# Kernel tuning notes

Hardware: AMD Instinct MI355X
Metric: run time of the kernel (lower is better)

Reference implementation:

```python
import jax, jax.numpy as jnp
import numpy as np
import math
from jax import lax

B, NP1, M, D, H, L, DFF = 16, 65, 256, 512, 8, 3, 2048
EPS_PROJ = 0.01  # MartingaleProjectionLayer is built with epsilon=0.01
LN_EPS = 1e-5


def _pos_encoding(n, d):
    pos = np.arange(n, dtype=np.float32)[:, None]
    div = np.exp(np.arange(0, d, 2, dtype=np.float32) * (-math.log(10000.0) / d))
    pe = np.zeros((n, d), dtype=np.float32)
    pe[:, 0::2] = np.sin(pos * div)
    pe[:, 1::2] = np.cos(pos * div)
    return jnp.asarray(pe)


def setup_inputs() -> dict:
    key = jax.random.key(0)
    ks = jax.random.split(key, 32)
    s = 0.02
    marg = jax.random.uniform(ks[0], (B, NP1, M), jnp.float32)
    marg = marg / marg.sum(axis=-1, keepdims=True)  # proper distributions
    return {
        "marginals": marg,
        "x_grid": jnp.linspace(-3.0, 3.0, M, dtype=jnp.float32),
        "conv_w": jax.random.normal(ks[1], (128, 1, 5), jnp.float32) * s,
        "conv_b": jax.random.normal(ks[2], (128,), jnp.float32) * s,
        "fc_w": jax.random.normal(ks[3], (128, D), jnp.float32) * s,
        "fc_b": jax.random.normal(ks[4], (D,), jnp.float32) * s,
        "ln0_g": jnp.ones((D,), jnp.float32),
        "ln0_b": jnp.zeros((D,), jnp.float32),
        "pos_enc": _pos_encoding(NP1, D),
        "qkv_w": jax.random.normal(ks[5], (L, 3 * D, D), jnp.float32) * s,
        "qkv_b": jax.random.normal(ks[6], (L, 3 * D), jnp.float32) * s,
        "out_w": jax.random.normal(ks[7], (L, D, D), jnp.float32) * s,
        "out_b": jax.random.normal(ks[8], (L, D), jnp.float32) * s,
        "ln1_g": jnp.ones((L, D), jnp.float32),
        "ln1_b": jnp.zeros((L, D), jnp.float32),
        "ff1_w": jax.random.normal(ks[9], (L, DFF, D), jnp.float32) * s,
        "ff1_b": jax.random.normal(ks[10], (L, DFF), jnp.float32) * s,
        "ff2_w": jax.random.normal(ks[11], (L, D, DFF), jnp.float32) * s,
        "ff2_b": jax.random.normal(ks[12], (L, D), jnp.float32) * s,
        "ln2_g": jnp.ones((L, D), jnp.float32),
        "ln2_b": jnp.zeros((L, D), jnp.float32),
        "u_w": jax.random.normal(ks[13], (M, D), jnp.float32) * s,
        "u_b": jax.random.normal(ks[14], (M,), jnp.float32) * s,
        "h_w": jax.random.normal(ks[15], (M, D), jnp.float32) * s,
        "h_b": jax.random.normal(ks[16], (M,), jnp.float32) * s,
    }


def _ln(x, g, b):
    mu = x.mean(axis=-1, keepdims=True)
    var = ((x - mu) ** 2).mean(axis=-1, keepdims=True)
    return (x - mu) * lax.rsqrt(var + LN_EPS) * g + b


def _gelu(x):
    return jax.nn.gelu(x, approximate=False)  # torch default exact GELU


def reference(marginals, x_grid, conv_w, conv_b, fc_w, fc_b, ln0_g, ln0_b,
              pos_enc, qkv_w, qkv_b, out_w, out_b, ln1_g, ln1_b,
              ff1_w, ff1_b, ff2_w, ff2_b, ln2_g, ln2_b, u_w, u_b, h_w, h_b):
    b, np1, m = marginals.shape
    n = np1 - 1
    d = fc_w.shape[1]
    nh = H
    dh = d // nh

    # ---- marginal embedding: Conv1d(1,128,k=5,pad=2) -> mean over grid -> FC+LN+GELU
    x = marginals.reshape(b * np1, 1, m)
    y = lax.conv_general_dilated(x, conv_w, (1,), [(2, 2)],
                                 dimension_numbers=("NCH", "OIH", "NCH"))
    y = y + conv_b[None, :, None]          # (b*np1, 128, m)
    emb = y.mean(axis=2)                   # (b*np1, 128)
    emb = _gelu(_ln(emb @ fc_w + fc_b, ln0_g, ln0_b))
    xs = emb.reshape(b, np1, d) + pos_enc[None, :np1, :]

    # ---- post-norm transformer encoder (dropout off / eval mode)
    scale = 1.0 / math.sqrt(dh)
    for l in range(L):
        qkv = xs @ qkv_w[l].T + qkv_b[l]                        # (b, s, 3d)
        q, k, v = jnp.split(qkv, 3, axis=-1)
        q = q.reshape(b, np1, nh, dh).transpose(0, 2, 1, 3)
        k = k.reshape(b, np1, nh, dh).transpose(0, 2, 1, 3)
        v = v.reshape(b, np1, nh, dh).transpose(0, 2, 1, 3)
        att = jax.nn.softmax(jnp.einsum("bhqd,bhkd->bhqk", q, k) * scale, axis=-1)
        o = jnp.einsum("bhqk,bhkd->bhqd", att, v)
        o = o.transpose(0, 2, 1, 3).reshape(b, np1, d)
        o = o @ out_w[l].T + out_b[l]
        xs = _ln(xs + o, ln1_g[l], ln1_b[l])
        ff = _gelu(xs @ ff1_w[l].T + ff1_b[l]) @ ff2_w[l].T + ff2_b[l]
        xs = _ln(xs + ff, ln2_g[l], ln2_b[l])

    u_pot = xs @ u_w.T + u_b                                    # (b, np1, M)
    h_raw = xs[:, :n, :] @ h_w.T + h_b                          # (b, n, M)

    # ---- vectorized martingale projection over all N timesteps
    x_diff = x_grid[:, None] - x_grid[None, :]                  # (M, M)
    h_kernel = h_raw[..., None] * x_diff                        # (b, n, M, M)
    P = jax.nn.softmax(h_kernel / EPS_PROJ, axis=-1)
    expected_next = jnp.einsum("bnij,j->bni", P, x_grid)
    drift = expected_next - x_grid                              # (b, n, M)
    mu = marginals[:, :n, :]
    weight_drift = (mu * drift).sum(axis=-1, keepdims=True)
    correction = weight_drift / (mu.sum(axis=-1, keepdims=True) + 1e-8)
    h_pot = h_raw - correction
    return (u_pot, h_pot)
```

## Files before the change

### kernel.cpp

```cpp
#include <hip/hip_runtime.h>
#include <math.h>


#define BT   1040
#define NP1  65
#define Dm   512
#define MG   256

typedef short short8 __attribute__((ext_vector_type(8)));
typedef float f32x4  __attribute__((ext_vector_type(4)));
typedef unsigned short u16;

__device__ __forceinline__ u16 f2bf(float f) {
  unsigned int u = __float_as_uint(f);
  u += 0x7FFF + ((u >> 16) & 1);
  return (u16)(u >> 16);
}

__device__ __forceinline__ float gelu_exact(float x) {
  return 0.5f * x * (1.0f + erff(x * 0.70710678118654752f));
}

__device__ __forceinline__ void async16(const u16* g, u16* l) {
  __builtin_amdgcn_global_load_lds(
      (const __attribute__((address_space(1))) unsigned int*)g,
      (__attribute__((address_space(3))) unsigned int*)l, 16, 0, 0);
}

__device__ __forceinline__ float wred(float v) {
#pragma unroll
  for (int o = 32; o; o >>= 1) v += __shfl_xor(v, o, 64);
  return v;
}

__device__ __forceinline__ float block_reduce_sum(float v, float* s) {
#pragma unroll
  for (int off = 32; off; off >>= 1) v += __shfl_down(v, off, 64);
  int lane = threadIdx.x & 63, wid = threadIdx.x >> 6;
  __syncthreads();
  if (lane == 0) s[wid] = v;
  __syncthreads();
  return s[0] + s[1] + s[2] + s[3];
}

__device__ __forceinline__ float f_closed(float a) {
  const float tf = 2.3529411765f;
  float t = a * tf;
  float s = fabsf(t);
  float E;
  if (s < 1e-4f) {
    E = 127.5f - 5461.25f * t;
  } else {
    float u = s * 256.0f;
    float term2 = (u < 80.0f) ? 256.0f / expm1f(u) : 0.0f;
    float Epos = 1.0f / expm1f(s) - term2;
    E = (t > 0.0f) ? Epos : 255.0f - Epos;
  }
  return -3.0f + 0.0235294118f * E;
}

__global__ __launch_bounds__(256) void prep_kernel(
    const float* __restrict__ qkv_w, const float* __restrict__ out_w,
    const float* __restrict__ ff1_w, const float* __restrict__ ff2_w,
    const float* __restrict__ u_w,   const float* __restrict__ h_w,
    u16* __restrict__ wdst,
    const float* __restrict__ marg, const float* __restrict__ conv_w,
    const float* __restrict__ conv_b, const float* __restrict__ fc_w,
    const float* __restrict__ fc_b, const float* __restrict__ g,
    const float* __restrict__ bb, const float* __restrict__ pos,
    float* __restrict__ xs, u16* __restrict__ xsb)
{
  const int tid = threadIdx.x;
  if (blockIdx.x < 512) {
    const size_t O1 = 2359296, O2 = 3145728, O3 = 6291456;
    const size_t O4 = 9437184, O5 = 9568256, TOT4 = 9699328 / 4;
    for (size_t e4 = (size_t)blockIdx.x * 256 + tid; e4 < TOT4;
         e4 += (size_t)512 * 256) {
      size_t e = e4 * 4;
      const float* src;
      if      (e < O1) src = qkv_w + e;
      else if (e < O2) src = out_w + (e - O1);
      else if (e < O3) src = ff1_w + (e - O2);
      else if (e < O4) src = ff2_w + (e - O3);
      else if (e < O5) src = u_w   + (e - O4);
      else             src = h_w   + (e - O5);
      float4 v = *(const float4*)src;
      unsigned int lo = (unsigned int)f2bf(v.x) | ((unsigned int)f2bf(v.y) << 16);
      unsigned int hi = (unsigned int)f2bf(v.z) | ((unsigned int)f2bf(v.w) << 16);
      *(uint2*)(wdst + e) = make_uint2(lo, hi);
    }
    return;
  }
  __shared__ float es[4][128];
  __shared__ float sS[4];
  __shared__ float edge[4][4];
  __shared__ float red[4];
  const int t0 = (blockIdx.x - 512) * 4;
  const int lane = tid & 63, wave = tid >> 6;
  {
    float4 mv = *(const float4*)(marg + (size_t)(t0 + wave) * MG + lane * 4);
    float S = wred(mv.x + mv.y + mv.z + mv.w);
    if (lane == 0) sS[wave] = S;
  }
  if (tid < 16) {
    int k = tid >> 2, e = tid & 3;
    int idx = (e < 2) ? e : (e + 252);
    edge[k][e] = marg[(size_t)(t0 + k) * MG + idx];
  }
  __syncthreads();
  if (tid < 128) {
    int o = tid;
    float w0 = conv_w[o*5+0], w1 = conv_w[o*5+1], w2 = conv_w[o*5+2];
    float w3 = conv_w[o*5+3], w4 = conv_w[o*5+4], cb = conv_b[o];
#pragma unroll
    for (int k = 0; k < 4; ++k) {
      float S = sS[k];
      float x0 = edge[k][0], x1 = edge[k][1], x254 = edge[k][2], x255 = edge[k][3];
      es[k][o] = (w0*(S - x254 - x255) + w1*(S - x255) + w2*S
                + w3*(S - x0) + w4*(S - x0 - x1)) * (1.0f/256.0f) + cb;
    }
  }
  __syncthreads();
  float b0 = fc_b[tid], b1 = fc_b[tid + 256];
  float z[4][2];
#pragma unroll
  for (int k = 0; k < 4; ++k) { z[k][0] = b0; z[k][1] = b1; }
#pragma unroll 4
  for (int o = 0; o < 128; ++o) {
    float f0 = fc_w[(size_t)o*Dm + tid];
    float f1 = fc_w[(size_t)o*Dm + tid + 256];
#pragma unroll
    for (int k = 0; k < 4; ++k) {
      float e = es[k][o];
      z[k][0] += e * f0; z[k][1] += e * f1;
    }
  }
  float g0 = g[tid], g1 = g[tid+256], e0 = bb[tid], e1 = bb[tid+256];
#pragma unroll
  for (int k = 0; k < 4; ++k) {
    float mu = block_reduce_sum(z[k][0] + z[k][1], red) * (1.0f/512.0f);
    float d0 = z[k][0] - mu, d1 = z[k][1] - mu;
    float var = block_reduce_sum(d0*d0 + d1*d1, red) * (1.0f/512.0f);
    float inv = rsqrtf(var + 1e-5f);
    int t = t0 + k, p = t % NP1;
    float y0 = gelu_exact(d0*inv*g0 + e0) + pos[(size_t)p*Dm + tid];
    float y1 = gelu_exact(d1*inv*g1 + e1) + pos[(size_t)p*Dm + tid + 256];
    xs[(size_t)t*Dm + tid]        = y0;
    xs[(size_t)t*Dm + tid + 256]  = y1;
    xsb[(size_t)t*Dm + tid]       = f2bf(y0);
    xsb[(size_t)t*Dm + tid + 256] = f2bf(y1);
  }
}

template<int SPLITS, int MODE>
__global__ __launch_bounds__(256) void gemm_mfma(
    const u16* __restrict__ A, const u16* __restrict__ Bw,
    const float* __restrict__ bias, float* __restrict__ Cf,
    u16* __restrict__ Cb, float* __restrict__ C2,
    const float* __restrict__ bias2, int Mrows, int N, int K)
{
  __shared__ u16 Asl[2][8*64*8];
  __shared__ u16 Bsl[2][8*64*8];
  const int tid = threadIdx.x;
  const int row0 = blockIdx.y * 64, col0 = blockIdx.x * 64;
  const int Ks = K / SPLITS, kbase = (int)blockIdx.z * Ks;
  const int lane = tid & 63, wave = tid >> 6;
  const int wm = (wave >> 1) * 32, wn = (wave & 1) * 32;
  const int l15 = lane & 15, q = lane >> 4;

  f32x4 acc[2][2];
  acc[0][0] = (f32x4){0,0,0,0}; acc[0][1] = (f32x4){0,0,0,0};
  acc[1][0] = (f32x4){0,0,0,0}; acc[1][1] = (f32x4){0,0,0,0};

  const int arow = min(row0 + lane, Mrows - 1);
  const size_t abase = (size_t)arow * K;
  const size_t bbase = (size_t)(col0 + lane) * K;
  const int c0w = wave * 2;

#pragma unroll
  for (int i = 0; i < 2; ++i) {
    int c = c0w + i;
    async16(A + abase + kbase + c * 8, &Asl[0][(size_t)(c * 64 + lane) * 8]);
    async16(Bw + bbase + kbase + c * 8, &Bsl[0][(size_t)(c * 64 + lane) * 8]);
  }

  const int nk = Ks >> 6;
  for (int t = 0; t < nk; ++t) {
    const int cur = t & 1;
    if (t + 1 < nk) {
      const int nxt = cur ^ 1;
      const int kk = kbase + (t + 1) * 64;
#pragma unroll
      for (int i = 0; i < 2; ++i) {
        int c = c0w + i;
        async16(A + abase + kk + c * 8, &Asl[nxt][(size_t)(c * 64 + lane) * 8]);
        async16(Bw + bbase + kk + c * 8, &Bsl[nxt][(size_t)(c * 64 + lane) * 8]);
      }
      asm volatile("s_waitcnt vmcnt(4)" ::: "memory");
    } else {
      asm volatile("s_waitcnt vmcnt(0)" ::: "memory");
    }
    __builtin_amdgcn_s_barrier();
#pragma unroll
    for (int tt = 0; tt < 2; ++tt) {
      int cc = tt * 4 + q;
      short8 af[2], bf[2];
#pragma unroll
      for (int mi = 0; mi < 2; ++mi)
        af[mi] = *(short8*)&Asl[cur][(size_t)(cc*64 + wm + mi*16 + l15) * 8];
#pragma unroll
      for (int ni = 0; ni < 2; ++ni)
        bf[ni] = *(short8*)&Bsl[cur][(size_t)(cc*64 + wn + ni*16 + l15) * 8];
#pragma unroll
      for (int mi = 0; mi < 2; ++mi)
#pragma unroll
        for (int ni = 0; ni < 2; ++ni)
          acc[mi][ni] = __builtin_amdgcn_mfma_f32_16x16x32_bf16(
              af[mi], bf[ni], acc[mi][ni], 0, 0, 0);
    }
    __builtin_amdgcn_s_barrier();
  }

  float* Cp = Cf;
  if (MODE == 2) Cp += (size_t)blockIdx.z * (size_t)Mrows * N;
#pragma unroll
  for (int mi = 0; mi < 2; ++mi) {
#pragma unroll
    for (int ni = 0; ni < 2; ++ni) {
      int col = col0 + wn + ni*16 + l15;
#pragma unroll
      for (int r = 0; r < 4; ++r) {
        int row = row0 + wm + mi*16 + q*4 + r;
        if (row < Mrows) {
          float v = acc[mi][ni][r];
          if (MODE == 0) {
            Cp[(size_t)row*N + col] = v + bias[col];
          } else if (MODE == 1) {
            Cb[(size_t)row*N + col] = f2bf(gelu_exact(v + bias[col]));
          } else if (MODE == 2) {
            Cp[(size_t)row*N + col] = v;
          } else {
            if (col < 256) Cf[(size_t)row*256 + col]         = v + bias[col];
            else           C2[(size_t)row*256 + (col - 256)] = v + bias2[col - 256];
          }
        }
      }
    }
  }
}

template<int S>
__global__ __launch_bounds__(256) void add_ln4(
    float* __restrict__ xs, u16* __restrict__ xsb,
    const float* __restrict__ part, const float* __restrict__ bias,
    const float* __restrict__ g, const float* __restrict__ bb)
{
  const int lane = threadIdx.x & 63, wave = threadIdx.x >> 6;
  const int t = blockIdx.x * 4 + wave;
  const int c0 = lane * 8;
  float* xp = xs + (size_t)t * Dm;
  float v[8];
  {
    float4 a0 = *(const float4*)(xp + c0), a1 = *(const float4*)(xp + c0 + 4);
    float4 b0 = *(const float4*)(bias + c0), b1 = *(const float4*)(bias + c0 + 4);
    v[0]=a0.x+b0.x; v[1]=a0.y+b0.y; v[2]=a0.z+b0.z; v[3]=a0.w+b0.w;
    v[4]=a1.x+b1.x; v[5]=a1.y+b1.y; v[6]=a1.z+b1.z; v[7]=a1.w+b1.w;
  }
#pragma unroll
  for (int s = 0; s < S; ++s) {
    const float* pp = part + (size_t)s*BT*Dm + (size_t)t*Dm + c0;
    float4 q0 = *(const float4*)pp, q1 = *(const float4*)(pp + 4);
    v[0]+=q0.x; v[1]+=q0.y; v[2]+=q0.z; v[3]+=q0.w;
    v[4]+=q1.x; v[5]+=q1.y; v[6]+=q1.z; v[7]+=q1.w;
  }
  float s1 = 0.f;
#pragma unroll
  for (int j = 0; j < 8; ++j) s1 += v[j];
  float mu = wred(s1) * (1.0f/512.0f);
  float s2 = 0.f;
#pragma unroll
  for (int j = 0; j < 8; ++j) { float d = v[j]-mu; s2 += d*d; }
  float inv = rsqrtf(wred(s2) * (1.0f/512.0f) + 1e-5f);
  float4 g0 = *(const float4*)(g + c0), g1 = *(const float4*)(g + c0 + 4);
  float4 e0 = *(const float4*)(bb + c0), e1 = *(const float4*)(bb + c0 + 4);
  float gg[8] = {g0.x,g0.y,g0.z,g0.w,g1.x,g1.y,g1.z,g1.w};
  float ee[8] = {e0.x,e0.y,e0.z,e0.w,e1.x,e1.y,e1.z,e1.w};
  float y[8]; u16 yb[8];
#pragma unroll
  for (int j = 0; j < 8; ++j) { y[j] = (v[j]-mu)*inv*gg[j] + ee[j]; yb[j] = f2bf(y[j]); }
  *(float4*)(xp + c0)     = make_float4(y[0],y[1],y[2],y[3]);
  *(float4*)(xp + c0 + 4) = make_float4(y[4],y[5],y[6],y[7]);
  *(short8*)(xsb + (size_t)t*Dm + c0) = *(short8*)yb;
}

__global__ __launch_bounds__(256) void attn_kernel(
    const float* __restrict__ qkv, u16* __restrict__ obufb)
{
  __shared__ float qv[65][67];
  __shared__ float ks[65][67];
  __shared__ float ss[65][67];
  const int b = blockIdx.x >> 3, h = blockIdx.x & 7;
  const int tid = threadIdx.x;
  const float* base = qkv + (size_t)b * NP1 * 1536 + h * 64;
  for (int idx = tid; idx < NP1 * 16; idx += 256) {
    int t = idx >> 4, c = (idx & 15) << 2;
    const float* p = base + (size_t)t * 1536 + c;
    float4 q4 = *(const float4*)(p);
    float4 k4 = *(const float4*)(p + 512);
    qv[t][c] = q4.x; qv[t][c+1] = q4.y; qv[t][c+2] = q4.z; qv[t][c+3] = q4.w;
    ks[t][c] = k4.x; ks[t][c+1] = k4.y; ks[t][c+2] = k4.z; ks[t][c+3] = k4.w;
  }
  __syncthreads();
#pragma unroll
  for (int it = 0; it < 2; ++it) {
    int tile = it * 256 + tid;
    if (tile < 289) {
      int ti = (tile / 17) * 4, tj = (tile % 17) * 4;
      const float* qr[4]; const float* kr[4];
#pragma unroll
      for (int i = 0; i < 4; ++i) { qr[i] = qv[min(ti + i, 64)]; kr[i] = ks[min(tj + i, 64)]; }
      float acc[4][4] = {};
      for (int d = 0; d < 64; ++d) {
        float a[4], bvv[4];
#pragma unroll
        for (int i = 0; i < 4; ++i) { a[i] = qr[i][d]; bvv[i] = kr[i][d]; }
#pragma unroll
        for (int i = 0; i < 4; ++i)
#pragma unroll
          for (int j = 0; j < 4; ++j) acc[i][j] += a[i] * bvv[j];
      }
#pragma unroll
      for (int i = 0; i < 4; ++i)
        if (ti + i < 65)
#pragma unroll
          for (int j = 0; j < 4; ++j)
            if (tj + j < 65) ss[ti + i][tj + j] = acc[i][j] * 0.125f;
    }
  }
  __syncthreads();
  for (int idx = tid; idx < NP1 * 16; idx += 256) {
    int t = idx >> 4, c = (idx & 15) << 2;
    float4 v4 = *(const float4*)(base + (size_t)t * 1536 + 1024 + c);
    qv[t][c] = v4.x; qv[t][c+1] = v4.y; qv[t][c+2] = v4.z; qv[t][c+3] = v4.w;
  }
  if (tid < 65) {
    float mx = -1e30f;
    for (int j = 0; j < 65; ++j) mx = fmaxf(mx, ss[tid][j]);
    float s = 0.0f;
    for (int j = 0; j < 65; ++j) { float e = expf(ss[tid][j] - mx); ss[tid][j] = e; s += e; }
    float inv = 1.0f / s;
    for (int j = 0; j < 65; ++j) ss[tid][j] *= inv;
  }
  __syncthreads();
#pragma unroll
  for (int it = 0; it < 2; ++it) {
    int tile = it * 256 + tid;
    if (tile < 272) {
      int ti = (tile >> 4) * 4, d0 = (tile & 15) * 4;
      const float* sr[4];
#pragma unroll
      for (int i = 0; i < 4; ++i) sr[i] = ss[min(ti + i, 64)];
      float acc[4][4] = {};
      for (int j = 0; j < 65; ++j) {
        float v0 = qv[j][d0], v1 = qv[j][d0+1], v2 = qv[j][d0+2], v3 = qv[j][d0+3];
#pragma unroll
        for (int i = 0; i < 4; ++i) {
          float s = sr[i][j];
          acc[i][0] += s * v0; acc[i][1] += s * v1;
          acc[i][2] += s * v2; acc[i][3] += s * v3;
        }
      }
#pragma unroll
      for (int i = 0; i < 4; ++i)
        if (ti + i < 65) {
          ushort4 o;
          o.x = f2bf(acc[i][0]); o.y = f2bf(acc[i][1]);
          o.z = f2bf(acc[i][2]); o.w = f2bf(acc[i][3]);
          *(ushort4*)(obufb + (size_t)(b * NP1 + ti + i) * Dm + h * 64 + d0) = o;
        }
    }
  }
}

__global__ __launch_bounds__(256) void proj_closed(
    const float* __restrict__ hbuf, const float* __restrict__ marg,
    const float* __restrict__ xg, float* __restrict__ out_h)
{
  const int tid = threadIdx.x, lane = tid & 63, wave = tid >> 6;
  const int rr = blockIdx.x * 4 + wave;
  const int b = rr >> 6, n = rr & 63;
  const int row = b * NP1 + n;
  const int i0 = lane * 4;
  float4 a4 = *(const float4*)(hbuf + (size_t)row * MG + i0);
  float4 x4 = *(const float4*)(xg + i0);
  float4 m4 = *(const float4*)(marg + (size_t)row * MG + i0);
  float av[4] = {a4.x, a4.y, a4.z, a4.w};
  float xv[4] = {x4.x, x4.y, x4.z, x4.w};
  float uv[4] = {m4.x, m4.y, m4.z, m4.w};
  float wd = 0.f, ms = 0.f;
#pragma unroll
  for (int k = 0; k < 4; ++k) {
    float drift = f_closed(av[k]) - xv[k];
    wd += uv[k] * drift; ms += uv[k];
  }
  wd = wred(wd); ms = wred(ms);
  float corr = wd / (ms + 1e-8f);
  *(float4*)(out_h + ((size_t)(b * 64 + n)) * MG + i0) =
      make_float4(av[0]-corr, av[1]-corr, av[2]-corr, av[3]-corr);
}

extern "C" void kernel_launch(void* const* d_in, const int* in_sizes, int n_in,
                              void* d_out, int out_size, void* d_ws, size_t ws_size,
                              hipStream_t stream)
{
  const float* marg   = (const float*)d_in[0];
  const float* xg     = (const float*)d_in[1];
  const float* conv_w = (const float*)d_in[2];
  const float* conv_b = (const float*)d_in[3];
  const float* fc_w   = (const float*)d_in[4];
  const float* fc_b   = (const float*)d_in[5];
  const float* ln0_g  = (const float*)d_in[6];
  const float* ln0_b  = (const float*)d_in[7];
  const float* pos    = (const float*)d_in[8];
  const float* qkv_w  = (const float*)d_in[9];
  const float* qkv_b  = (const float*)d_in[10];
  const float* out_w  = (const float*)d_in[11];
  const float* out_b  = (const float*)d_in[12];
  const float* ln1_g  = (const float*)d_in[13];
  const float* ln1_b  = (const float*)d_in[14];
  const float* ff1_w  = (const float*)d_in[15];
  const float* ff1_b  = (const float*)d_in[16];
  const float* ff2_w  = (const float*)d_in[17];
  const float* ff2_b  = (const float*)d_in[18];
  const float* ln2_g  = (const float*)d_in[19];
  const float* ln2_b  = (const float*)d_in[20];
  const float* u_w    = (const float*)d_in[21];
  const float* u_b    = (const float*)d_in[22];
  const float* h_w    = (const float*)d_in[23];
  const float* h_b    = (const float*)d_in[24];
  float* out = (float*)d_out;

  float* ws = (float*)d_ws;
  float* xs      = ws;
  float* qkvbuf  = ws + 532480;
  float* part    = ws + 2129920;
  float* hbuf    = ws + 4259840;
  u16*   xsb     = (u16*)(ws + 4526080);
  u16*   obufb   = (u16*)(ws + 4792320);
  u16*   ffb     = (u16*)(ws + 5058560);
  u16*   wbf     = (u16*)(ws + 6123520);

  const u16* qkv_bw = wbf;
  const u16* out_bw = wbf + 2359296;
  const u16* ff1_bw = wbf + 3145728;
  const u16* ff2_bw = wbf + 6291456;
  const u16* uh_bw  = wbf + 9437184;

  prep_kernel<<<772, 256, 0, stream>>>(
      qkv_w, out_w, ff1_w, ff2_w, u_w, h_w, wbf,
      marg, conv_w, conv_b, fc_w, fc_b, ln0_g, ln0_b, pos, xs, xsb);

  for (int l = 0; l < 3; ++l) {
    gemm_mfma<1,0><<<dim3(24, 17), 256, 0, stream>>>(
        xsb, qkv_bw + (size_t)l*786432, qkv_b + l*1536, qkvbuf,
        nullptr, nullptr, nullptr, BT, 1536, 512);
    attn_kernel<<<128, 256, 0, stream>>>(qkvbuf, obufb);
    gemm_mfma<2,2><<<dim3(8, 17, 2), 256, 0, stream>>>(
        obufb, out_bw + (size_t)l*262144, nullptr, part,
        nullptr, nullptr, nullptr, BT, 512, 512);
    add_ln4<2><<<260, 256, 0, stream>>>(xs, xsb, part, out_b + l*512,
                                        ln1_g + l*512, ln1_b + l*512);
    gemm_mfma<1,1><<<dim3(32, 17), 256, 0, stream>>>(
        xsb, ff1_bw + (size_t)l*1048576, ff1_b + l*2048, nullptr,
        ffb, nullptr, nullptr, BT, 2048, 512);
    gemm_mfma<4,2><<<dim3(8, 17, 4), 256, 0, stream>>>(
        ffb, ff2_bw + (size_t)l*1048576, nullptr, part,
        nullptr, nullptr, nullptr, BT, 512, 2048);
    add_ln4<4><<<260, 256, 0, stream>>>(xs, xsb, part, ff2_b + l*512,
                                        ln2_g + l*512, ln2_b + l*512);
  }

  gemm_mfma<1,3><<<dim3(8, 17), 256, 0, stream>>>(
      xsb, uh_bw, u_b, out, nullptr, hbuf, h_b, BT, 512, 512);
  proj_closed<<<256, 256, 0, stream>>>(hbuf, marg, xg, out + 1040*256);
}
```

Baseline: 405.4 us.

## Fuse all stages into one persistent cooperative kernel with grid syncs

Replaces the chain of about 23 separate kernel launches (prep, per-layer GEMMs, attention, add+LN, final projection) with a single persistent cooperative kernel. Each stage's work becomes a device function run over a grid-stride job loop, and the stages are separated by grid.sync. The aim is to remove launch overhead and inter-kernel gaps, at the cost of grid-barrier latency, a grid capped at 544 blocks (occupancy-derived, up to 2 per CU, at least 64), and a shared LDS buffer sized for the largest stage that may lower occupancy.

```diff
diff --git a/kernel.cpp b/kernel.cpp
--- a/kernel.cpp
+++ b/kernel.cpp
@@ -1,5 +1,8 @@
 #include <hip/hip_runtime.h>
+#include <hip/hip_cooperative_groups.h>
 #include <math.h>
+
+namespace cg = cooperative_groups;
 
 
 #define BT   1040
@@ -59,83 +62,87 @@
   return -3.0f + 0.0235294118f * E;
 }
 
-__global__ __launch_bounds__(256) void prep_kernel(
-    const float* __restrict__ qkv_w, const float* __restrict__ out_w,
-    const float* __restrict__ ff1_w, const float* __restrict__ ff2_w,
-    const float* __restrict__ u_w,   const float* __restrict__ h_w,
-    u16* __restrict__ wdst,
-    const float* __restrict__ marg, const float* __restrict__ conv_w,
-    const float* __restrict__ conv_b, const float* __restrict__ fc_w,
-    const float* __restrict__ fc_b, const float* __restrict__ g,
-    const float* __restrict__ bb, const float* __restrict__ pos,
-    float* __restrict__ xs, u16* __restrict__ xsb)
-{
-  const int tid = threadIdx.x;
-  if (blockIdx.x < 512) {
-    const size_t O1 = 2359296, O2 = 3145728, O3 = 6291456;
-    const size_t O4 = 9437184, O5 = 9568256, TOT4 = 9699328 / 4;
-    for (size_t e4 = (size_t)blockIdx.x * 256 + tid; e4 < TOT4;
-         e4 += (size_t)512 * 256) {
-      size_t e = e4 * 4;
-      const float* src;
-      if      (e < O1) src = qkv_w + e;
-      else if (e < O2) src = out_w + (e - O1);
-      else if (e < O3) src = ff1_w + (e - O2);
-      else if (e < O4) src = ff2_w + (e - O3);
-      else if (e < O5) src = u_w   + (e - O4);
-      else             src = h_w   + (e - O5);
-      float4 v = *(const float4*)src;
-      unsigned int lo = (unsigned int)f2bf(v.x) | ((unsigned int)f2bf(v.y) << 16);
-      unsigned int hi = (unsigned int)f2bf(v.z) | ((unsigned int)f2bf(v.w) << 16);
-      *(uint2*)(wdst + e) = make_uint2(lo, hi);
-    }
-    return;
-  }
-  __shared__ float es[4][128];
-  __shared__ float sS[4];
-  __shared__ float edge[4][4];
-  __shared__ float red[4];
-  const int t0 = (blockIdx.x - 512) * 4;
-  const int lane = tid & 63, wave = tid >> 6;
+struct MegaArgs {
+  const float *marg, *xg, *conv_w, *conv_b, *fc_w, *fc_b, *ln0_g, *ln0_b, *pos;
+  const float *qkv_b, *out_b, *ln1_g, *ln1_b, *ff1_b, *ff2_b, *ln2_g, *ln2_b;
+  const float *u_b, *h_b;
+  const float *qkv_w, *out_w, *ff1_w, *ff2_w, *u_w, *h_w;
+  float *out, *xs, *qkvbuf, *part, *hbuf;
+  u16 *xsb, *obufb, *ffb, *wbf;
+};
+
+
+__device__ __forceinline__ void convert_weights(
+    int bid, int half, const MegaArgs& a)
+{
+  const size_t O1 = 2359296, O2 = 3145728, O3 = 6291456;
+  const size_t O4 = 9437184, O5 = 9568256, TOT4 = 9699328 / 4;
+  for (size_t e4 = (size_t)bid * 256 + threadIdx.x; e4 < TOT4;
+       e4 += (size_t)half * 256) {
+    size_t e = e4 * 4;
+    const float* src;
+    if      (e < O1) src = a.qkv_w + e;
+    else if (e < O2) src = a.out_w + (e - O1);
+    else if (e < O3) src = a.ff1_w + (e - O2);
+    else if (e < O4) src = a.ff2_w + (e - O3);
+    else if (e < O5) src = a.u_w   + (e - O4);
+    else             src = a.h_w   + (e - O5);
+    float4 v = *(const float4*)src;
+    unsigned int lo = (unsigned int)f2bf(v.x) | ((unsigned int)f2bf(v.y) << 16);
+    unsigned int hi = (unsigned int)f2bf(v.z) | ((unsigned int)f2bf(v.w) << 16);
+    *(uint2*)(a.wbf + e) = make_uint2(lo, hi);
+  }
+}
+
+__device__ __forceinline__ void embed_job(int j, const MegaArgs& a, float* smem)
+{
+  float* es   = smem;
+  float* sS   = smem + 512;
+  float* edge = smem + 516;
+  float* red  = smem + 532;
+  const int tid = threadIdx.x, lane = tid & 63, wave = tid >> 6;
+  const int t0 = j * 4;
+  __syncthreads();
   {
-    float4 mv = *(const float4*)(marg + (size_t)(t0 + wave) * MG + lane * 4);
+    float4 mv = *(const float4*)(a.marg + (size_t)(t0 + wave) * MG + lane * 4);
     float S = wred(mv.x + mv.y + mv.z + mv.w);
     if (lane == 0) sS[wave] = S;
   }
   if (tid < 16) {
     int k = tid >> 2, e = tid & 3;
     int idx = (e < 2) ? e : (e + 252);
-    edge[k][e] = marg[(size_t)(t0 + k) * MG + idx];
+    edge[k * 4 + e] = a.marg[(size_t)(t0 + k) * MG + idx];
   }
   __syncthreads();
   if (tid < 128) {
     int o = tid;
-    float w0 = conv_w[o*5+0], w1 = conv_w[o*5+1], w2 = conv_w[o*5+2];
-    float w3 = conv_w[o*5+3], w4 = conv_w[o*5+4], cb = conv_b[o];
+    float w0 = a.conv_w[o*5+0], w1 = a.conv_w[o*5+1], w2 = a.conv_w[o*5+2];
+    float w3 = a.conv_w[o*5+3], w4 = a.conv_w[o*5+4], cb = a.conv_b[o];
 #pragma unroll
     for (int k = 0; k < 4; ++k) {
       float S = sS[k];
-      float x0 = edge[k][0], x1 = edge[k][1], x254 = edge[k][2], x255 = edge[k][3];
-      es[k][o] = (w0*(S - x254 - x255) + w1*(S - x255) + w2*S
-                + w3*(S - x0) + w4*(S - x0 - x1)) * (1.0f/256.0f) + cb;
-    }
-  }
-  __syncthreads();
-  float b0 = fc_b[tid], b1 = fc_b[tid + 256];
+      float x0 = edge[k*4+0], x1 = edge[k*4+1], x254 = edge[k*4+2], x255 = edge[k*4+3];
+      es[k*128 + o] = (w0*(S - x254 - x255) + w1*(S - x255) + w2*S
+                     + w3*(S - x0) + w4*(S - x0 - x1)) * (1.0f/256.0f) + cb;
+    }
+  }
+  __syncthreads();
+  float b0 = a.fc_b[tid], b1 = a.fc_b[tid + 256];
   float z[4][2];
 #pragma unroll
   for (int k = 0; k < 4; ++k) { z[k][0] = b0; z[k][1] = b1; }
 #pragma unroll 4
   for (int o = 0; o < 128; ++o) {
-    float f0 = fc_w[(size_t)o*Dm + tid];
-    float f1 = fc_w[(size_t)o*Dm + tid + 256];
+    float f0 = a.fc_w[(size_t)o*Dm + tid];
+    float f1 = a.fc_w[(size_t)o*Dm + tid + 256];
 #pragma unroll
     for (int k = 0; k < 4; ++k) {
-      float e = es[k][o];
+      float e = es[k*128 + o];
       z[k][0] += e * f0; z[k][1] += e * f1;
     }
   }
-  float g0 = g[tid], g1 = g[tid+256], e0 = bb[tid], e1 = bb[tid+256];
+  float g0 = a.ln0_g[tid], g1 = a.ln0_g[tid+256];
+  float e0 = a.ln0_b[tid], e1 = a.ln0_b[tid+256];
 #pragma unroll
   for (int k = 0; k < 4; ++k) {
     float mu = block_reduce_sum(z[k][0] + z[k][1], red) * (1.0f/512.0f);
@@ -143,30 +150,31 @@
     float var = block_reduce_sum(d0*d0 + d1*d1, red) * (1.0f/512.0f);
     float inv = rsqrtf(var + 1e-5f);
     int t = t0 + k, p = t % NP1;
-    float y0 = gelu_exact(d0*inv*g0 + e0) + pos[(size_t)p*Dm + tid];
-    float y1 = gelu_exact(d1*inv*g1 + e1) + pos[(size_t)p*Dm + tid + 256];
-    xs[(size_t)t*Dm + tid]        = y0;
-    xs[(size_t)t*Dm + tid + 256]  = y1;
-    xsb[(size_t)t*Dm + tid]       = f2bf(y0);
-    xsb[(size_t)t*Dm + tid + 256] = f2bf(y1);
+    float y0 = gelu_exact(d0*inv*g0 + e0) + a.pos[(size_t)p*Dm + tid];
+    float y1 = gelu_exact(d1*inv*g1 + e1) + a.pos[(size_t)p*Dm + tid + 256];
+    a.xs[(size_t)t*Dm + tid]        = y0;
+    a.xs[(size_t)t*Dm + tid + 256]  = y1;
+    a.xsb[(size_t)t*Dm + tid]       = f2bf(y0);
+    a.xsb[(size_t)t*Dm + tid + 256] = f2bf(y1);
   }
 }
 
 template<int SPLITS, int MODE>
-__global__ __launch_bounds__(256) void gemm_mfma(
+__device__ __forceinline__ void gemm_tile(
     const u16* __restrict__ A, const u16* __restrict__ Bw,
     const float* __restrict__ bias, float* __restrict__ Cf,
     u16* __restrict__ Cb, float* __restrict__ C2,
-    const float* __restrict__ bias2, int Mrows, int N, int K)
-{
-  __shared__ u16 Asl[2][8*64*8];
-  __shared__ u16 Bsl[2][8*64*8];
+    const float* __restrict__ bias2, int Mrows, int N, int K,
+    int bx, int by, int bz, u16* Asl, u16* Bsl)
+{
   const int tid = threadIdx.x;
-  const int row0 = blockIdx.y * 64, col0 = blockIdx.x * 64;
-  const int Ks = K / SPLITS, kbase = (int)blockIdx.z * Ks;
+  const int row0 = by * 64, col0 = bx * 64;
+  const int Ks = K / SPLITS, kbase = bz * Ks;
   const int lane = tid & 63, wave = tid >> 6;
   const int wm = (wave >> 1) * 32, wn = (wave & 1) * 32;
   const int l15 = lane & 15, q = lane >> 4;
+
+  __syncthreads();
 
   f32x4 acc[2][2];
   acc[0][0] = (f32x4){0,0,0,0}; acc[0][1] = (f32x4){0,0,0,0};
@@ -180,8 +188,8 @@
 #pragma unroll
   for (int i = 0; i < 2; ++i) {
     int c = c0w + i;
-    async16(A + abase + kbase + c * 8, &Asl[0][(size_t)(c * 64 + lane) * 8]);
-    async16(Bw + bbase + kbase + c * 8, &Bsl[0][(size_t)(c * 64 + lane) * 8]);
+    async16(A + abase + kbase + c * 8, Asl + (size_t)(c * 64 + lane) * 8);
+    async16(Bw + bbase + kbase + c * 8, Bsl + (size_t)(c * 64 + lane) * 8);
   }
 
   const int nk = Ks >> 6;
@@ -193,8 +201,8 @@
 #pragma unroll
       for (int i = 0; i < 2; ++i) {
         int c = c0w + i;
-        async16(A + abase + kk + c * 8, &Asl[nxt][(size_t)(c * 64 + lane) * 8]);
-        async16(Bw + bbase + kk + c * 8, &Bsl[nxt][(size_t)(c * 64 + lane) * 8]);
+        async16(A + abase + kk + c * 8, Asl + nxt*4096 + (size_t)(c*64 + lane)*8);
+        async16(Bw + bbase + kk + c * 8, Bsl + nxt*4096 + (size_t)(c*64 + lane)*8);
       }
       asm volatile("s_waitcnt vmcnt(4)" ::: "memory");
     } else {
@@ -207,10 +215,10 @@
       short8 af[2], bf[2];
 #pragma unroll
       for (int mi = 0; mi < 2; ++mi)
-        af[mi] = *(short8*)&Asl[cur][(size_t)(cc*64 + wm + mi*16 + l15) * 8];
+        af[mi] = *(short8*)(Asl + cur*4096 + (size_t)(cc*64 + wm + mi*16 + l15) * 8);
 #pragma unroll
       for (int ni = 0; ni < 2; ++ni)
-        bf[ni] = *(short8*)&Bsl[cur][(size_t)(cc*64 + wn + ni*16 + l15) * 8];
+        bf[ni] = *(short8*)(Bsl + cur*4096 + (size_t)(cc*64 + wn + ni*16 + l15) * 8);
 #pragma unroll
       for (int mi = 0; mi < 2; ++mi)
 #pragma unroll
@@ -222,7 +230,7 @@
   }
 
   float* Cp = Cf;
-  if (MODE == 2) Cp += (size_t)blockIdx.z * (size_t)Mrows * N;
+  if (MODE == 2) Cp += (size_t)bz * (size_t)Mrows * N;
 #pragma unroll
   for (int mi = 0; mi < 2; ++mi) {
 #pragma unroll
@@ -249,14 +257,104 @@
   }
 }
 
+__device__ __forceinline__ void attn_job(int jj, const float* __restrict__ qkv,
+                                         u16* __restrict__ obufb, float* smem)
+{
+  float (*qv)[67] = (float (*)[67])smem;
+  float (*ks)[67] = (float (*)[67])(smem + 4355);
+  float (*ss)[67] = (float (*)[67])(smem + 8710);
+  const int b = jj >> 3, h = jj & 7;
+  const int tid = threadIdx.x;
+  const float* base = qkv + (size_t)b * NP1 * 1536 + h * 64;
+  __syncthreads();
+  for (int idx = tid; idx < NP1 * 16; idx += 256) {
+    int t = idx >> 4, c = (idx & 15) << 2;
+    const float* p = base + (size_t)t * 1536 + c;
+    float4 q4 = *(const float4*)(p);
+    float4 k4 = *(const float4*)(p + 512);
+    qv[t][c] = q4.x; qv[t][c+1] = q4.y; qv[t][c+2] = q4.z; qv[t][c+3] = q4.w;
+    ks[t][c] = k4.x; ks[t][c+1] = k4.y; ks[t][c+2] = k4.z; ks[t][c+3] = k4.w;
+  }
+  __syncthreads();
+#pragma unroll
+  for (int it = 0; it < 2; ++it) {
+    int tile = it * 256 + tid;
+    if (tile < 289) {
+      int ti = (tile / 17) * 4, tj = (tile % 17) * 4;
+      const float* qr[4]; const float* kr[4];
+#pragma unroll
+      for (int i = 0; i < 4; ++i) { qr[i] = qv[min(ti + i, 64)]; kr[i] = ks[min(tj + i, 64)]; }
+      float acc[4][4] = {};
+      for (int d = 0; d < 64; ++d) {
+        float aa[4], bvv[4];
+#pragma unroll
+        for (int i = 0; i < 4; ++i) { aa[i] = qr[i][d]; bvv[i] = kr[i][d]; }
+#pragma unroll
+        for (int i = 0; i < 4; ++i)
+#pragma unroll
+          for (int j = 0; j < 4; ++j) acc[i][j] += aa[i] * bvv[j];
+      }
+#pragma unroll
+      for (int i = 0; i < 4; ++i)
+        if (ti + i < 65)
+#pragma unroll
+          for (int j = 0; j < 4; ++j)
+            if (tj + j < 65) ss[ti + i][tj + j] = acc[i][j] * 0.125f;
+    }
+  }
+  __syncthreads();
+  for (int idx = tid; idx < NP1 * 16; idx += 256) {
+    int t = idx >> 4, c = (idx & 15) << 2;
+    float4 v4 = *(const float4*)(base + (size_t)t * 1536 + 1024 + c);
+    qv[t][c] = v4.x; qv[t][c+1] = v4.y; qv[t][c+2] = v4.z; qv[t][c+3] = v4.w;
+  }
+  if (tid < 65) {
+    float mx = -1e30f;
+    for (int j = 0; j < 65; ++j) mx = fmaxf(mx, ss[tid][j]);
+    float s = 0.0f;
+    for (int j = 0; j < 65; ++j) { float e = expf(ss[tid][j] - mx); ss[tid][j] = e; s += e; }
+    float inv = 1.0f / s;
+    for (int j = 0; j < 65; ++j) ss[tid][j] *= inv;
+  }
+  __syncthreads();
+#pragma unroll
+  for (int it = 0; it < 2; ++it) {
+    int tile = it * 256 + tid;
+    if (tile < 272) {
+      int ti = (tile >> 4) * 4, d0 = (tile & 15) * 4;
+      const float* sr[4];
+#pragma unroll
+      for (int i = 0; i < 4; ++i) sr[i] = ss[min(ti + i, 64)];
+      float acc[4][4] = {};
+      for (int j = 0; j < 65; ++j) {
+        float v0 = qv[j][d0], v1 = qv[j][d0+1], v2 = qv[j][d0+2], v3 = qv[j][d0+3];
+#pragma unroll
+        for (int i = 0; i < 4; ++i) {
+          float s = sr[i][j];
+          acc[i][0] += s * v0; acc[i][1] += s * v1;
+          acc[i][2] += s * v2; acc[i][3] += s * v3;
+        }
+      }
+#pragma unroll
+      for (int i = 0; i < 4; ++i)
+        if (ti + i < 65) {
+          ushort4 o;
+          o.x = f2bf(acc[i][0]); o.y = f2bf(acc[i][1]);
+          o.z = f2bf(acc[i][2]); o.w = f2bf(acc[i][3]);
+          *(ushort4*)(obufb + (size_t)(b * NP1 + ti + i) * Dm + h * 64 + d0) = o;
+        }
+    }
+  }
+}
+
 template<int S>
-__global__ __launch_bounds__(256) void add_ln4(
-    float* __restrict__ xs, u16* __restrict__ xsb,
-    const float* __restrict__ part, const float* __restrict__ bias,
-    const float* __restrict__ g, const float* __restrict__ bb)
+__device__ __forceinline__ void addln_job(int j, float* __restrict__ xs,
+    u16* __restrict__ xsb, const float* __restrict__ part,
+    const float* __restrict__ bias, const float* __restrict__ g,
+    const float* __restrict__ bb)
 {
   const int lane = threadIdx.x & 63, wave = threadIdx.x >> 6;
-  const int t = blockIdx.x * 4 + wave;
+  const int t = j * 4 + wave;
   const int c0 = lane * 8;
   float* xp = xs + (size_t)t * Dm;
   float v[8];
@@ -275,11 +373,11 @@
   }
   float s1 = 0.f;
 #pragma unroll
-  for (int j = 0; j < 8; ++j) s1 += v[j];
+  for (int jj = 0; jj < 8; ++jj) s1 += v[jj];
   float mu = wred(s1) * (1.0f/512.0f);
   float s2 = 0.f;
 #pragma unroll
-  for (int j = 0; j < 8; ++j) { float d = v[j]-mu; s2 += d*d; }
+  for (int jj = 0; jj < 8; ++jj) { float d = v[jj]-mu; s2 += d*d; }
   float inv = rsqrtf(wred(s2) * (1.0f/512.0f) + 1e-5f);
   float4 g0 = *(const float4*)(g + c0), g1 = *(const float4*)(g + c0 + 4);
   float4 e0 = *(const float4*)(bb + c0), e1 = *(const float4*)(bb + c0 + 4);
@@ -287,107 +385,18 @@
   float ee[8] = {e0.x,e0.y,e0.z,e0.w,e1.x,e1.y,e1.z,e1.w};
   float y[8]; u16 yb[8];
 #pragma unroll
-  for (int j = 0; j < 8; ++j) { y[j] = (v[j]-mu)*inv*gg[j] + ee[j]; yb[j] = f2bf(y[j]); }
+  for (int jj = 0; jj < 8; ++jj) { y[jj] = (v[jj]-mu)*inv*gg[jj] + ee[jj]; yb[jj] = f2bf(y[jj]); }
   *(float4*)(xp + c0)     = make_float4(y[0],y[1],y[2],y[3]);
   *(float4*)(xp + c0 + 4) = make_float4(y[4],y[5],y[6],y[7]);
   *(short8*)(xsb + (size_t)t*Dm + c0) = *(short8*)yb;
 }
 
-__global__ __launch_bounds__(256) void attn_kernel(
-    const float* __restrict__ qkv, u16* __restrict__ obufb)
-{
-  __shared__ float qv[65][67];
-  __shared__ float ks[65][67];
-  __shared__ float ss[65][67];
-  const int b = blockIdx.x >> 3, h = blockIdx.x & 7;
-  const int tid = threadIdx.x;
-  const float* base = qkv + (size_t)b * NP1 * 1536 + h * 64;
-  for (int idx = tid; idx < NP1 * 16; idx += 256) {
-    int t = idx >> 4, c = (idx & 15) << 2;
-    const float* p = base + (size_t)t * 1536 + c;
-    float4 q4 = *(const float4*)(p);
-    float4 k4 = *(const float4*)(p + 512);
-    qv[t][c] = q4.x; qv[t][c+1] = q4.y; qv[t][c+2] = q4.z; qv[t][c+3] = q4.w;
-    ks[t][c] = k4.x; ks[t][c+1] = k4.y; ks[t][c+2] = k4.z; ks[t][c+3] = k4.w;
-  }
-  __syncthreads();
-#pragma unroll
-  for (int it = 0; it < 2; ++it) {
-    int tile = it * 256 + tid;
-    if (tile < 289) {
-      int ti = (tile / 17) * 4, tj = (tile % 17) * 4;
-      const float* qr[4]; const float* kr[4];
-#pragma unroll
-      for (int i = 0; i < 4; ++i) { qr[i] = qv[min(ti + i, 64)]; kr[i] = ks[min(tj + i, 64)]; }
-      float acc[4][4] = {};
-      for (int d = 0; d < 64; ++d) {
-        float a[4], bvv[4];
-#pragma unroll
-        for (int i = 0; i < 4; ++i) { a[i] = qr[i][d]; bvv[i] = kr[i][d]; }
-#pragma unroll
-        for (int i = 0; i < 4; ++i)
-#pragma unroll
-          for (int j = 0; j < 4; ++j) acc[i][j] += a[i] * bvv[j];
-      }
-#pragma unroll
-      for (int i = 0; i < 4; ++i)
-        if (ti + i < 65)
-#pragma unroll
-          for (int j = 0; j < 4; ++j)
-            if (tj + j < 65) ss[ti + i][tj + j] = acc[i][j] * 0.125f;
-    }
-  }
-  __syncthreads();
-  for (int idx = tid; idx < NP1 * 16; idx += 256) {
-    int t = idx >> 4, c = (idx & 15) << 2;
-    float4 v4 = *(const float4*)(base + (size_t)t * 1536 + 1024 + c);
-    qv[t][c] = v4.x; qv[t][c+1] = v4.y; qv[t][c+2] = v4.z; qv[t][c+3] = v4.w;
-  }
-  if (tid < 65) {
-    float mx = -1e30f;
-    for (int j = 0; j < 65; ++j) mx = fmaxf(mx, ss[tid][j]);
-    float s = 0.0f;
-    for (int j = 0; j < 65; ++j) { float e = expf(ss[tid][j] - mx); ss[tid][j] = e; s += e; }
-    float inv = 1.0f / s;
-    for (int j = 0; j < 65; ++j) ss[tid][j] *= inv;
-  }
-  __syncthreads();
-#pragma unroll
-  for (int it = 0; it < 2; ++it) {
-    int tile = it * 256 + tid;
-    if (tile < 272) {
-      int ti = (tile >> 4) * 4, d0 = (tile & 15) * 4;
-      const float* sr[4];
-#pragma unroll
-      for (int i = 0; i < 4; ++i) sr[i] = ss[min(ti + i, 64)];
-      float acc[4][4] = {};
-      for (int j = 0; j < 65; ++j) {
-        float v0 = qv[j][d0], v1 = qv[j][d0+1], v2 = qv[j][d0+2], v3 = qv[j][d0+3];
-#pragma unroll
-        for (int i = 0; i < 4; ++i) {
-          float s = sr[i][j];
-          acc[i][0] += s * v0; acc[i][1] += s * v1;
-          acc[i][2] += s * v2; acc[i][3] += s * v3;
-        }
-      }
-#pragma unroll
-      for (int i = 0; i < 4; ++i)
-        if (ti + i < 65) {
-          ushort4 o;
-          o.x = f2bf(acc[i][0]); o.y = f2bf(acc[i][1]);
-          o.z = f2bf(acc[i][2]); o.w = f2bf(acc[i][3]);
-          *(ushort4*)(obufb + (size_t)(b * NP1 + ti + i) * Dm + h * 64 + d0) = o;
-        }
-    }
-  }
-}
-
-__global__ __launch_bounds__(256) void proj_closed(
-    const float* __restrict__ hbuf, const float* __restrict__ marg,
-    const float* __restrict__ xg, float* __restrict__ out_h)
+__device__ __forceinline__ void proj_job(int j, const float* __restrict__ hbuf,
+    const float* __restrict__ marg, const float* __restrict__ xg,
+    float* __restrict__ out_h)
 {
   const int tid = threadIdx.x, lane = tid & 63, wave = tid >> 6;
-  const int rr = blockIdx.x * 4 + wave;
+  const int rr = j * 4 + wave;
   const int b = rr >> 6, n = rr & 63;
   const int row = b * NP1 + n;
   const int i0 = lane * 4;
@@ -409,78 +418,127 @@
       make_float4(av[0]-corr, av[1]-corr, av[2]-corr, av[3]-corr);
 }
 
+__global__ __launch_bounds__(256, 2) void mega(MegaArgs a)
+{
+  cg::grid_group grid = cg::this_grid();
+  __shared__ alignas(16) float smem[13072];
+  const int bid = blockIdx.x;
+  const int nb  = gridDim.x;
+  u16* Asl = (u16*)smem;
+  u16* Bsl = (u16*)smem + 8192;
+
+  {
+    int half = nb >> 1;
+    if (bid < half) {
+      convert_weights(bid, half, a);
+    } else {
+      for (int j = bid - half; j < 260; j += nb - half)
+        embed_job(j, a, smem);
+    }
+  }
+  grid.sync();
+
+  for (int l = 0; l < 3; ++l) {
+    const u16* qw  = a.wbf + (size_t)l * 786432;
+    const u16* ow  = a.wbf + 2359296 + (size_t)l * 262144;
+    const u16* f1w = a.wbf + 3145728 + (size_t)l * 1048576;
+    const u16* f2w = a.wbf + 6291456 + (size_t)l * 1048576;
+
+    for (int j = bid; j < 408; j += nb)
+      gemm_tile<1,0>(a.xsb, qw, a.qkv_b + l*1536, a.qkvbuf, nullptr, nullptr,
+                     nullptr, BT, 1536, 512, j % 24, j / 24, 0, Asl, Bsl);
+    grid.sync();
+
+    for (int j = bid; j < 128; j += nb)
+      attn_job(j, a.qkvbuf, a.obufb, smem);
+    grid.sync();
+
+    for (int j = bid; j < 272; j += nb)
+      gemm_tile<2,2>(a.obufb, ow, nullptr, a.part, nullptr, nullptr, nullptr,
+                     BT, 512, 512, j % 8, (j / 8) % 17, j / 136, Asl, Bsl);
+    grid.sync();
+
+    for (int j = bid; j < 260; j += nb)
+      addln_job<2>(j, a.xs, a.xsb, a.part, a.out_b + l*512,
+                   a.ln1_g + l*512, a.ln1_b + l*512);
+    grid.sync();
+
+    for (int j = bid; j < 544; j += nb)
+      gemm_tile<1,1>(a.xsb, f1w, a.ff1_b + l*2048, nullptr, a.ffb, nullptr,
+                     nullptr, BT, 2048, 512, j % 32, j / 32, 0, Asl, Bsl);
+    grid.sync();
+
+    for (int j = bid; j < 544; j += nb)
+      gemm_tile<4,2>(a.ffb, f2w, nullptr, a.part, nullptr, nullptr, nullptr,
+                     BT, 512, 2048, j % 8, (j / 8) % 17, j / 136, Asl, Bsl);
+    grid.sync();
+
+    for (int j = bid; j < 260; j += nb)
+      addln_job<4>(j, a.xs, a.xsb, a.part, a.ff2_b + l*512,
+                   a.ln2_g + l*512, a.ln2_b + l*512);
+    grid.sync();
+  }
+
+  const u16* uhw = a.wbf + 9437184;
+  for (int j = bid; j < 136; j += nb)
+    gemm_tile<1,3>(a.xsb, uhw, a.u_b, a.out, nullptr, a.hbuf, a.h_b,
+                   BT, 512, 512, j % 8, j / 8, 0, Asl, Bsl);
+  grid.sync();
+
+  for (int j = bid; j < 256; j += nb)
+    proj_job(j, a.hbuf, a.marg, a.xg, a.out + 1040 * 256);
+}
+
 extern "C" void kernel_launch(void* const* d_in, const int* in_sizes, int n_in,
                               void* d_out, int out_size, void* d_ws, size_t ws_size,
                               hipStream_t stream)
 {
-  const float* marg   = (const float*)d_in[0];
-  const float* xg     = (const float*)d_in[1];
-  const float* conv_w = (const float*)d_in[2];
-  const float* conv_b = (const float*)d_in[3];
-  const float* fc_w   = (const float*)d_in[4];
-  const float* fc_b   = (const float*)d_in[5];
-  const float* ln0_g  = (const float*)d_in[6];
-  const float* ln0_b  = (const float*)d_in[7];
-  const float* pos    = (const float*)d_in[8];
-  const float* qkv_w  = (const float*)d_in[9];
-  const float* qkv_b  = (const float*)d_in[10];
-  const float* out_w  = (const float*)d_in[11];
-  const float* out_b  = (const float*)d_in[12];
-  const float* ln1_g  = (const float*)d_in[13];
-  const float* ln1_b  = (const float*)d_in[14];
-  const float* ff1_w  = (const float*)d_in[15];
-  const float* ff1_b  = (const float*)d_in[16];
-  const float* ff2_w  = (const float*)d_in[17];
-  const float* ff2_b  = (const float*)d_in[18];
-  const float* ln2_g  = (const float*)d_in[19];
-  const float* ln2_b  = (const float*)d_in[20];
-  const float* u_w    = (const float*)d_in[21];
-  const float* u_b    = (const float*)d_in[22];
-  const float* h_w    = (const float*)d_in[23];
-  const float* h_b    = (const float*)d_in[24];
-  float* out = (float*)d_out;
-
   float* ws = (float*)d_ws;
-  float* xs      = ws;
-  float* qkvbuf  = ws + 532480;
-  float* part    = ws + 2129920;
-  float* hbuf    = ws + 4259840;
-  u16*   xsb     = (u16*)(ws + 4526080);
-  u16*   obufb   = (u16*)(ws + 4792320);
-  u16*   ffb     = (u16*)(ws + 5058560);
-  u16*   wbf     = (u16*)(ws + 6123520);
-
-  const u16* qkv_bw = wbf;
-  const u16* out_bw = wbf + 2359296;
-  const u16* ff1_bw = wbf + 3145728;
-  const u16* ff2_bw = wbf + 6291456;
-  const u16* uh_bw  = wbf + 9437184;
-
-  prep_kernel<<<772, 256, 0, stream>>>(
-      qkv_w, out_w, ff1_w, ff2_w, u_w, h_w, wbf,
-      marg, conv_w, conv_b, fc_w, fc_b, ln0_g, ln0_b, pos, xs, xsb);
-
-  for (int l = 0; l < 3; ++l) {
-    gemm_mfma<1,0><<<dim3(24, 17), 256, 0, stream>>>(
-        xsb, qkv_bw + (size_t)l*786432, qkv_b + l*1536, qkvbuf,
-        nullptr, nullptr, nullptr, BT, 1536, 512);
-    attn_kernel<<<128, 256, 0, stream>>>(qkvbuf, obufb);
-    gemm_mfma<2,2><<<dim3(8, 17, 2), 256, 0, stream>>>(
-        obufb, out_bw + (size_t)l*262144, nullptr, part,
-        nullptr, nullptr, nullptr, BT, 512, 512);
-    add_ln4<2><<<260, 256, 0, stream>>>(xs, xsb, part, out_b + l*512,
-                                        ln1_g + l*512, ln1_b + l*512);
-    gemm_mfma<1,1><<<dim3(32, 17), 256, 0, stream>>>(
-        xsb, ff1_bw + (size_t)l*1048576, ff1_b + l*2048, nullptr,
-        ffb, nullptr, nullptr, BT, 2048, 512);
-    gemm_mfma<4,2><<<dim3(8, 17, 4), 256, 0, stream>>>(
-        ffb, ff2_bw + (size_t)l*1048576, nullptr, part,
-        nullptr, nullptr, nullptr, BT, 512, 2048);
-    add_ln4<4><<<260, 256, 0, stream>>>(xs, xsb, part, ff2_b + l*512,
-                                        ln2_g + l*512, ln2_b + l*512);
-  }
-
-  gemm_mfma<1,3><<<dim3(8, 17), 256, 0, stream>>>(
-      xsb, uh_bw, u_b, out, nullptr, hbuf, h_b, BT, 512, 512);
-  proj_closed<<<256, 256, 0, stream>>>(hbuf, marg, xg, out + 1040*256);
-}
+
+  MegaArgs a;
+  a.marg   = (const float*)d_in[0];
+  a.xg     = (const float*)d_in[1];
+  a.conv_w = (const float*)d_in[2];
+  a.conv_b = (const float*)d_in[3];
+  a.fc_w   = (const float*)d_in[4];
+  a.fc_b   = (const float*)d_in[5];
+  a.ln0_g  = (const float*)d_in[6];
+  a.ln0_b  = (const float*)d_in[7];
+  a.pos    = (const float*)d_in[8];
+  a.qkv_w  = (const float*)d_in[9];
+  a.qkv_b  = (const float*)d_in[10];
+  a.out_w  = (const float*)d_in[11];
+  a.out_b  = (const float*)d_in[12];
+  a.ln1_g  = (const float*)d_in[13];
+  a.ln1_b  = (const float*)d_in[14];
+  a.ff1_w  = (const float*)d_in[15];
+  a.ff1_b  = (const float*)d_in[16];
+  a.ff2_w  = (const float*)d_in[17];
+  a.ff2_b  = (const float*)d_in[18];
+  a.ln2_g  = (const float*)d_in[19];
+  a.ln2_b  = (const float*)d_in[20];
+  a.u_w    = (const float*)d_in[21];
+  a.u_b    = (const float*)d_in[22];
+  a.h_w    = (const float*)d_in[23];
+  a.h_b    = (const float*)d_in[24];
+  a.out    = (float*)d_out;
+
+  a.xs     = ws;
+  a.qkvbuf = ws + 532480;
+  a.part   = ws + 2129920;
+  a.hbuf   = ws + 4259840;
+  a.xsb    = (u16*)(ws + 4526080);
+  a.obufb  = (u16*)(ws + 4792320);
+  a.ffb    = (u16*)(ws + 5058560);
+  a.wbf    = (u16*)(ws + 6123520);
+
+  int nblk = 0;
+  hipOccupancyMaxActiveBlocksPerMultiprocessor(&nblk, mega, 256, 0);
+  if (nblk < 1) nblk = 1;
+  int gridsz = nblk * 256;
+  if (gridsz > 544) gridsz = 544;
+  if (gridsz < 64)  gridsz = 64;
+
+  void* kargs[] = { (void*)&a };
+  hipLaunchCooperativeKernel(mega, dim3(gridsz), dim3(256), kargs, 0, stream);
+}
```

Result: slower. 1.072 ms (+164.5%).
